# Kernel optimization log

Hardware: AMD Instinct MI355X
Metric: run time of the kernel (lower is better)

Reference implementation:

```python
import jax, jax.numpy as jnp
import numpy as np

N_ATOMS = 131072
N_EDGES = 524288
N_MOLS = 2048
D = 128      # n_atom_basis
F = 128      # n_filters
G = 50       # n_gaussians
T = 3        # interaction blocks
CUTOFF = 5.0
LOG2 = float(np.log(2.0))


def ssp(x):
    # shifted softplus: ln(0.5*e^x + 0.5) = softplus(x) - ln 2
    return jax.nn.softplus(x) - LOG2


def setup_inputs() -> dict:
    key = jax.random.key(0)
    ks = jax.random.split(key, 20)
    s = 0.05
    z = jax.random.randint(ks[0], (N_ATOMS,), 1, 100, dtype=jnp.int32)
    xyz = jax.random.normal(ks[1], (N_ATOMS, 3), dtype=jnp.float32) * 3.0
    a0 = jax.random.randint(ks[2], (N_EDGES,), 0, N_ATOMS, dtype=jnp.int32)
    off = jax.random.randint(ks[3], (N_EDGES,), 1, N_ATOMS, dtype=jnp.int32)
    a = jnp.stack([a0, (a0 + off) % N_ATOMS], axis=1)  # distinct endpoints
    mol_id = jnp.sort(jax.random.randint(ks[4], (N_ATOMS,), 0, N_MOLS, dtype=jnp.int32))
    emb = (jax.random.normal(ks[5], (100, D)) * s).at[0].set(0.0)  # padding_idx=0
    return dict(
        xyz=xyz,
        emb=emb,
        fw1=jax.random.normal(ks[6], (T, G, F)) * s,
        fb1=jnp.zeros((T, F)),
        fw2=jax.random.normal(ks[7], (T, F, F)) * s,
        fb2=jnp.zeros((T, F)),
        win=jax.random.normal(ks[8], (T, D, F)) * s,
        wout1=jax.random.normal(ks[9], (T, F, D)) * s,
        bout1=jnp.zeros((T, D)),
        wout2=jax.random.normal(ks[10], (T, D, D)) * s,
        bout2=jnp.zeros((T, D)),
        wa1=jax.random.normal(ks[11], (D, D // 2)) * s,
        ba1=jnp.zeros((D // 2,)),
        wa2=jax.random.normal(ks[12], (D // 2, 1)) * s,
        ba2=jnp.zeros((1,)),
        z=z, a=a, mol_id=mol_id,
    )


def reference(xyz, emb, fw1, fb1, fw2, fb2, win, wout1, bout1, wout2, bout2,
              wa1, ba1, wa2, ba2, z, a, mol_id):
    r = emb[z]                                            # [N, D] atom embeddings
    # edge distances: e = ||xyz[a0] - xyz[a1]||  -> [E, 1]
    d = jnp.sqrt(((xyz[a[:, 0]] - xyz[a[:, 1]]) ** 2).sum(-1))[:, None]
    # Gaussian smearing on [0, cutoff]
    offsets = jnp.linspace(0.0, CUTOFF, G)
    width = offsets[1] - offsets[0]
    g = jnp.exp((-0.5 / width ** 2) * (d - offsets) ** 2)  # [E, G]
    # smooth cosine cutoff (cutoff_soft)
    C = 0.5 * (jnp.cos(d * jnp.pi / CUTOFF) + 1.0)          # [E, 1]
    for t in range(T):
        # continuous filter network on edge features
        W = ssp(g @ fw1[t] + fb1[t]) @ fw2[t] + fb2[t]      # [E, F]
        W = W * C
        h = r @ win[t]                                      # in2f, no bias [N, F]
        # symmetric gather-filter-scatter over undirected edge list
        y = jnp.zeros_like(h)
        y = y.at[a[:, 0]].add(h[a[:, 1]] * W)
        y = y.at[a[:, 1]].add(h[a[:, 0]] * W)
        dr = ssp(y @ wout1[t] + bout1[t]) @ wout2[t] + bout2[t]
        r = r + dr                                          # residual update
    # atomwise energy head
    r = ssp(r @ wa1 + ba1) @ wa2 + ba2                      # [N, 1]
    # per-molecule sum pooling (torch.split + sum)
    return jax.ops.segment_sum(r, mol_id, num_segments=N_MOLS)  # [N_MOLS, 1]
```

## Files before the change

kernel.cpp:

```cpp
#include <hip/hip_runtime.h>
#include <hip/hip_bf16.h>

#define N_ATOMS 131072
#define N_EDGES 524288
#define N_MOLS  2048
#define DD      128
#define FF      128
#define GG      50
#define TT      3

typedef __hip_bfloat16 bf16;
typedef __attribute__((ext_vector_type(8))) short short8;
typedef __attribute__((ext_vector_type(4))) float floatx4;

__device__ __forceinline__ float b2f(bf16 v) { return __bfloat162float(v); }
__device__ __forceinline__ bf16  f2b(float v) { return __float2bfloat16(v); }

__device__ __forceinline__ unsigned short f2bu(float f) {
    unsigned u = __float_as_uint(f);
    u += 0x7fff + ((u >> 16) & 1);
    return (unsigned short)(u >> 16);
}
__device__ __forceinline__ bf16 f2b_fast(float f) {
    union { unsigned short u; bf16 b; } c; c.u = f2bu(f); return c.b;
}
__device__ __forceinline__ unsigned int pk2(float lo, float hi) {
    return ((unsigned)f2bu(hi) << 16) | f2bu(lo);
}

__device__ __forceinline__ unsigned short b2us(bf16 v) {
    union { bf16 b; unsigned short u; } c; c.b = v; return c.u;
}

__device__ __forceinline__ float2 up2(unsigned int u) {
    float2 f;
    f.x = __uint_as_float(u << 16);
    f.y = __uint_as_float(u & 0xffff0000u);
    return f;
}

__device__ __forceinline__ float sspf(float x) {
    float e = __expf(-fabsf(x));
    return fmaxf(x, 0.f) + __logf(1.f + e) - 0.69314718056f;
}

template <int NCT>
__device__ __forceinline__ void mfma_half(const bf16* A, const bf16* B,
                                          floatx4 (&acc)[2][NCT],
                                          int kA, int wave, int q, int ln) {
#pragma unroll
    for (int k0 = 0; k0 < 64; k0 += 32) {
        short8 a0 = *(const short8*)(A + (wave * 32 + ln) * 136 + kA + k0 + q * 8);
        short8 a1 = *(const short8*)(A + (wave * 32 + 16 + ln) * 136 + kA + k0 + q * 8);
#pragma unroll
        for (int ct = 0; ct < NCT; ct++) {
            short8 b = *(const short8*)(B + (ct * 16 + ln) * 72 + k0 + q * 8);
            acc[0][ct] = __builtin_amdgcn_mfma_f32_16x16x32_bf16(a0, b, acc[0][ct], 0, 0, 0);
            acc[1][ct] = __builtin_amdgcn_mfma_f32_16x16x32_bf16(a1, b, acc[1][ct], 0, 0, 0);
        }
    }
}

template <int NCT>
__device__ __forceinline__ void mfma64(const bf16* A, const bf16* B,
                                       floatx4 (&acc)[NCT],
                                       int kA, int wave, int q, int ln) {
#pragma unroll
    for (int k0 = 0; k0 < 64; k0 += 32) {
        short8 a = *(const short8*)(A + (wave * 16 + ln) * 136 + kA + k0 + q * 8);
#pragma unroll
        for (int ct = 0; ct < NCT; ct++) {
            short8 b = *(const short8*)(B + (ct * 16 + ln) * 72 + k0 + q * 8);
            acc[ct] = __builtin_amdgcn_mfma_f32_16x16x32_bf16(a, b, acc[ct], 0, 0, 0);
        }
    }
}

__device__ __forceinline__ void stage_b(bf16* B, const bf16* WT, int k0,
                                        int nrows, int ldk, int tid) {
    for (int i = tid; i < nrows * 8; i += 256) {
        int n = i >> 3, kc = i & 7;
        *(short8*)(B + n * 72 + kc * 8) =
            *(const short8*)(WT + n * ldk + k0 + kc * 8);
    }
}

__global__ __launch_bounds__(256) void k_init(const float* __restrict__ emb,
                                              const int* __restrict__ z,
                                              float* __restrict__ r) {
    int idx = blockIdx.x * 256 + threadIdx.x;
    int atom = idx >> 7, col = idx & 127;
    r[idx] = emb[z[atom] * DD + col];
}

__global__ __launch_bounds__(256) void k_dist(const float* __restrict__ xyz,
                                              const int* __restrict__ a,
                                              float* __restrict__ dArr,
                                              float* __restrict__ cArr,
                                              float* __restrict__ molE) {
    int e = blockIdx.x * 256 + threadIdx.x;
    if (e < N_MOLS) molE[e] = 0.f;
    int A0 = a[2 * e], A1 = a[2 * e + 1];
    float dx = xyz[3 * A0]     - xyz[3 * A1];
    float dy = xyz[3 * A0 + 1] - xyz[3 * A1 + 1];
    float dz = xyz[3 * A0 + 2] - xyz[3 * A1 + 2];
    float d = sqrtf(dx * dx + dy * dy + dz * dz);
    dArr[e] = d;
    cArr[e] = 0.5f * (__cosf(d * 0.6283185307179586f) + 1.f);
}

__global__ __launch_bounds__(256) void k_wt(const float* __restrict__ fw1,
                                            const float* __restrict__ fw2,
                                            const float* __restrict__ win,
                                            const float* __restrict__ wout1,
                                            const float* __restrict__ wout2,
                                            const float* __restrict__ wa1,
                                            bf16* __restrict__ fw1T, bf16* __restrict__ fw2T,
                                            bf16* __restrict__ winT, bf16* __restrict__ wout1T,
                                            bf16* __restrict__ wout2T, bf16* __restrict__ wa1T) {
    int idx = blockIdx.x * 256 + threadIdx.x;
    if (idx < 3 * 128 * 64) {
        int t = idx / 8192, j = idx % 8192;
        int n = j >> 6, k = j & 63;
        fw1T[idx] = (k < GG) ? f2b(fw1[t * GG * FF + k * FF + n]) : f2b(0.f);
        return;
    }
    idx -= 3 * 128 * 64;
    if (idx < 3 * 16384) { int t = idx / 16384, j = idx % 16384; int n = j >> 7, k = j & 127;
        fw2T[idx] = f2b(fw2[t * 16384 + k * 128 + n]); return; }
    idx -= 3 * 16384;
    if (idx < 3 * 16384) { int t = idx / 16384, j = idx % 16384; int n = j >> 7, k = j & 127;
        winT[idx] = f2b(win[t * 16384 + k * 128 + n]); return; }
    idx -= 3 * 16384;
    if (idx < 3 * 16384) { int t = idx / 16384, j = idx % 16384; int n = j >> 7, k = j & 127;
        wout1T[idx] = f2b(wout1[t * 16384 + k * 128 + n]); return; }
    idx -= 3 * 16384;
    if (idx < 3 * 16384) { int t = idx / 16384, j = idx % 16384; int n = j >> 7, k = j & 127;
        wout2T[idx] = f2b(wout2[t * 16384 + k * 128 + n]); return; }
    idx -= 3 * 16384;
    if (idx < 64 * 128) { int n = idx >> 7, k = idx & 127;
        wa1T[idx] = f2b(wa1[k * 64 + n]); return; }
}

__global__ __launch_bounds__(256) void k_zero(int* __restrict__ p, int n) {
    int i = blockIdx.x * 256 + threadIdx.x;
    if (i < n) p[i] = 0;
}

__global__ __launch_bounds__(256) void k_count(const int* __restrict__ a,
                                               int* __restrict__ counts) {
    int e = blockIdx.x * 256 + threadIdx.x;
    atomicAdd(&counts[a[2 * e]], 1);
    atomicAdd(&counts[a[2 * e + 1]], 1);
}

__global__ __launch_bounds__(256) void k_scan(int* __restrict__ counts,
                                              int* __restrict__ ptr) {
    __shared__ int part[256];
    int tid = threadIdx.x;
    const int CH = N_ATOMS / 256;
    int base = tid * CH;
    int s = 0;
    for (int i = 0; i < CH; i++) s += counts[base + i];
    part[tid] = s;
    __syncthreads();
    if (tid == 0) {
        int acc = 0;
        for (int i = 0; i < 256; i++) { int v = part[i]; part[i] = acc; acc += v; }
    }
    __syncthreads();
    int run = part[tid];
    for (int i = 0; i < CH; i++) {
        int v = counts[base + i];
        ptr[base + i] = run;
        counts[base + i] = run;
        run += v;
    }
    if (tid == 255) ptr[N_ATOMS] = run;
}

__global__ __launch_bounds__(256) void k_fill(const int* __restrict__ a,
                                              int* __restrict__ cursor,
                                              int* __restrict__ adj) {
    int e = blockIdx.x * 256 + threadIdx.x;
    int A0 = a[2 * e], A1 = a[2 * e + 1];
    int p0 = atomicAdd(&cursor[A0], 1);
    adj[2 * p0] = e; adj[2 * p0 + 1] = A1;
    int p1 = atomicAdd(&cursor[A1], 1);
    adj[2 * p1] = e; adj[2 * p1 + 1] = A0;
}


__global__ __launch_bounds__(256, 4) void k_h64(const float* __restrict__ r,
                                                const bf16* __restrict__ winT_t,
                                                bf16* __restrict__ h) {
    __shared__ __align__(16) bf16 A[64][136];
    __shared__ __align__(16) bf16 B[128][72];
    int tid = threadIdx.x, n0 = blockIdx.x * 64;
    for (int i = tid; i < 64 * 32; i += 256) {
        int row = i >> 5, c4 = (i & 31) * 4;
        float4 v = *(const float4*)(r + (size_t)(n0 + row) * DD + c4);
        uint2 p; p.x = pk2(v.x, v.y); p.y = pk2(v.z, v.w);
        *(uint2*)(&A[row][c4]) = p;
    }
    stage_b(&B[0][0], winT_t, 0, 128, 128, tid);
    __syncthreads();
    int wave = tid >> 6, lane = tid & 63, q = lane >> 4, ln = lane & 15;
    floatx4 acc[8];
#pragma unroll
    for (int j = 0; j < 8; j++) acc[j] = (floatx4){0.f, 0.f, 0.f, 0.f};
    mfma64<8>(&A[0][0], &B[0][0], acc, 0, wave, q, ln);
    __syncthreads();
    stage_b(&B[0][0], winT_t, 64, 128, 128, tid);
    __syncthreads();
    mfma64<8>(&A[0][0], &B[0][0], acc, 64, wave, q, ln);
#pragma unroll
    for (int ct = 0; ct < 8; ct++)
#pragma unroll
        for (int rg = 0; rg < 4; rg++) {
            int row = wave * 16 + q * 4 + rg, col = ct * 16 + ln;
            A[row][col] = f2b_fast(acc[ct][rg]);
        }
    __syncthreads();
    for (int i = tid; i < 64 * 16; i += 256) {
        int row = i >> 4, seg = i & 15;
        *(uint4*)(h + (size_t)(n0 + row) * FF + seg * 8) =
            *(const uint4*)(&A[row][seg * 8]);
    }
}

__global__ __launch_bounds__(256, 4) void k_edge_w64(const float* __restrict__ dArr,
                                                     const float* __restrict__ cArr,
                                                     const bf16* __restrict__ fw1T_t,
                                                     const float* __restrict__ fb1_t,
                                                     const bf16* __restrict__ fw2T_t,
                                                     const float* __restrict__ fb2_t,
                                                     bf16* __restrict__ Wt) {
    __shared__ __align__(16) bf16 A[64][136];
    __shared__ __align__(16) bf16 B[128][72];
    __shared__ float dS[64], cS[64], b1S[128], b2S[128];
    int tid = threadIdx.x, e0 = blockIdx.x * 64;
    if (tid < 64) { dS[tid] = dArr[e0 + tid]; cS[tid] = cArr[e0 + tid]; }
    if (tid < 128) { b1S[tid] = fb1_t[tid]; b2S[tid] = fb2_t[tid]; }
    stage_b(&B[0][0], fw1T_t, 0, 128, 64, tid);
    __syncthreads();
    const float width = 5.0f / 49.0f;
    const float coeff = -0.5f / (width * width);
    for (int idx = tid; idx < 64 * 32; idx += 256) {
        int i = idx >> 5, kp = (idx & 31) * 2;
        float d = dS[i];
        float t0 = d - (float)kp * width;
        float t1 = d - (float)(kp + 1) * width;
        float v0 = (kp < GG)     ? __expf(coeff * t0 * t0) : 0.f;
        float v1 = (kp + 1 < GG) ? __expf(coeff * t1 * t1) : 0.f;
        *(unsigned int*)(&A[i][kp]) = pk2(v0, v1);
    }
    __syncthreads();
    int wave = tid >> 6, lane = tid & 63, q = lane >> 4, ln = lane & 15;
    floatx4 acc[8];
#pragma unroll
    for (int j = 0; j < 8; j++) acc[j] = (floatx4){0.f, 0.f, 0.f, 0.f};
    mfma64<8>(&A[0][0], &B[0][0], acc, 0, wave, q, ln);
#pragma unroll
    for (int ct = 0; ct < 8; ct++)
#pragma unroll
        for (int rg = 0; rg < 4; rg++) {
            int row = wave * 16 + q * 4 + rg, col = ct * 16 + ln;
            A[row][col] = f2b_fast(sspf(acc[ct][rg] + b1S[col]));
        }
    __syncthreads();
    stage_b(&B[0][0], fw2T_t, 0, 128, 128, tid);
    __syncthreads();
#pragma unroll
    for (int j = 0; j < 8; j++) acc[j] = (floatx4){0.f, 0.f, 0.f, 0.f};
    mfma64<8>(&A[0][0], &B[0][0], acc, 0, wave, q, ln);
    __syncthreads();
    stage_b(&B[0][0], fw2T_t, 64, 128, 128, tid);
    __syncthreads();
    mfma64<8>(&A[0][0], &B[0][0], acc, 64, wave, q, ln);
#pragma unroll
    for (int ct = 0; ct < 8; ct++)
#pragma unroll
        for (int rg = 0; rg < 4; rg++) {
            int row = wave * 16 + q * 4 + rg, col = ct * 16 + ln;
            A[row][col] = f2b_fast((acc[ct][rg] + b2S[col]) * cS[row]);
        }
    __syncthreads();
    for (int i = tid; i < 64 * 16; i += 256) {
        int row = i >> 4, seg = i & 15;
        *(uint4*)(Wt + (size_t)(e0 + row) * FF + seg * 8) =
            *(const uint4*)(&A[row][seg * 8]);
    }
}

__global__ __launch_bounds__(256, 4) void k_gather_node64(const int* __restrict__ ptr,
                                                          const int* __restrict__ adj,
                                                          const bf16* __restrict__ Wt,
                                                          const bf16* __restrict__ h,
                                                          const bf16* __restrict__ wout1T_t,
                                                          const float* __restrict__ bo1_t,
                                                          const bf16* __restrict__ wout2T_t,
                                                          const float* __restrict__ bo2_t,
                                                          float* __restrict__ r) {
    __shared__ __align__(16) bf16 A[64][136];
    __shared__ __align__(16) bf16 B[128][72];
    __shared__ float b1S[128], b2S[128];
    int tid = threadIdx.x, n0 = blockIdx.x * 64;
    if (tid < 128) { b1S[tid] = bo1_t[tid]; b2S[tid] = bo2_t[tid]; }
    int wave = tid >> 6, lane = tid & 63;
    int seg = lane & 15;
    int rg  = lane >> 4;
    for (int k = 0; k < 16; k++) {
        int row = wave * 16 + k;
        int atom = n0 + row;
        int beg = ptr[atom], end = ptr[atom + 1];
        float ac[8];
#pragma unroll
        for (int j = 0; j < 8; j++) ac[j] = 0.f;
        for (int s0 = beg; s0 < end; s0 += 4) {
            int slot = s0 + rg;
            if (slot < end) {
                int2 eo = *(const int2*)(adj + 2 * slot);
                uint4 wv = *(const uint4*)(Wt + (size_t)eo.x * FF + seg * 8);
                uint4 hv = *(const uint4*)(h + (size_t)eo.y * FF + seg * 8);
                float2 w0 = up2(wv.x), h0 = up2(hv.x);
                float2 w1 = up2(wv.y), h1 = up2(hv.y);
                float2 w2 = up2(wv.z), h2 = up2(hv.z);
                float2 w3 = up2(wv.w), h3 = up2(hv.w);
                ac[0] = fmaf(w0.x, h0.x, ac[0]); ac[1] = fmaf(w0.y, h0.y, ac[1]);
                ac[2] = fmaf(w1.x, h1.x, ac[2]); ac[3] = fmaf(w1.y, h1.y, ac[3]);
                ac[4] = fmaf(w2.x, h2.x, ac[4]); ac[5] = fmaf(w2.y, h2.y, ac[5]);
                ac[6] = fmaf(w3.x, h3.x, ac[6]); ac[7] = fmaf(w3.y, h3.y, ac[7]);
            }
        }
#pragma unroll
        for (int j = 0; j < 8; j++) {
            float v = ac[j];
            v += __shfl_down(v, 32);
            v += __shfl_down(v, 16);
            ac[j] = v;
        }
        if (rg == 0) {
            uint4 o;
            o.x = pk2(ac[0], ac[1]);
            o.y = pk2(ac[2], ac[3]);
            o.z = pk2(ac[4], ac[5]);
            o.w = pk2(ac[6], ac[7]);
            *(uint4*)(&A[row][seg * 8]) = o;
        }
    }
    stage_b(&B[0][0], wout1T_t, 0, 128, 128, tid);
    __syncthreads();
    int q = lane >> 4, ln = lane & 15;
    floatx4 acc[8];
#pragma unroll
    for (int j = 0; j < 8; j++) acc[j] = (floatx4){0.f, 0.f, 0.f, 0.f};
    mfma64<8>(&A[0][0], &B[0][0], acc, 0, wave, q, ln);
    __syncthreads();
    stage_b(&B[0][0], wout1T_t, 64, 128, 128, tid);
    __syncthreads();
    mfma64<8>(&A[0][0], &B[0][0], acc, 64, wave, q, ln);
#pragma unroll
    for (int ct = 0; ct < 8; ct++)
#pragma unroll
        for (int rgi = 0; rgi < 4; rgi++) {
            int row = wave * 16 + q * 4 + rgi, col = ct * 16 + ln;
            A[row][col] = f2b_fast(sspf(acc[ct][rgi] + b1S[col]));
        }
    __syncthreads();
    stage_b(&B[0][0], wout2T_t, 0, 128, 128, tid);
    __syncthreads();
#pragma unroll
    for (int j = 0; j < 8; j++) acc[j] = (floatx4){0.f, 0.f, 0.f, 0.f};
    mfma64<8>(&A[0][0], &B[0][0], acc, 0, wave, q, ln);
    __syncthreads();
    stage_b(&B[0][0], wout2T_t, 64, 128, 128, tid);
    __syncthreads();
    mfma64<8>(&A[0][0], &B[0][0], acc, 64, wave, q, ln);
#pragma unroll
    for (int ct = 0; ct < 8; ct++)
#pragma unroll
        for (int rgi = 0; rgi < 4; rgi++) {
            int row = wave * 16 + q * 4 + rgi, col = ct * 16 + ln;
            size_t off = (size_t)(n0 + row) * DD + col;
            r[off] += acc[ct][rgi] + b2S[col];
        }
}

__global__ __launch_bounds__(256) void k_h(const float* __restrict__ r,
                                           const bf16* __restrict__ winT_t,
                                           bf16* __restrict__ h,
                                           float* __restrict__ y) {
    __shared__ __align__(16) bf16 A[128][136];
    __shared__ __align__(16) bf16 B[128][72];
    int tid = threadIdx.x, n0 = blockIdx.x * 128;
    for (int i = tid; i < 128 * 32; i += 256) {
        int row = i >> 5, c4 = (i & 31) * 4;
        float4 v = *(const float4*)(r + (size_t)(n0 + row) * DD + c4);
        A[row][c4]     = f2b(v.x);
        A[row][c4 + 1] = f2b(v.y);
        A[row][c4 + 2] = f2b(v.z);
        A[row][c4 + 3] = f2b(v.w);
        *(float4*)(y + (size_t)(n0 + row) * FF + c4) = (float4){0.f, 0.f, 0.f, 0.f};
    }
    stage_b(&B[0][0], winT_t, 0, 128, 128, tid);
    __syncthreads();
    int wave = tid >> 6, lane = tid & 63, q = lane >> 4, ln = lane & 15;
    floatx4 acc[2][8];
#pragma unroll
    for (int i = 0; i < 2; i++)
#pragma unroll
        for (int j = 0; j < 8; j++) acc[i][j] = (floatx4){0.f, 0.f, 0.f, 0.f};
    mfma_half<8>(&A[0][0], &B[0][0], acc, 0, wave, q, ln);
    __syncthreads();
    stage_b(&B[0][0], winT_t, 64, 128, 128, tid);
    __syncthreads();
    mfma_half<8>(&A[0][0], &B[0][0], acc, 64, wave, q, ln);
#pragma unroll
    for (int rt = 0; rt < 2; rt++)
#pragma unroll
        for (int ct = 0; ct < 8; ct++)
#pragma unroll
            for (int rg = 0; rg < 4; rg++) {
                int row = wave * 32 + rt * 16 + q * 4 + rg, col = ct * 16 + ln;
                h[(size_t)(n0 + row) * FF + col] = f2b(acc[rt][ct][rg]);
            }
}

__global__ __launch_bounds__(256) void k_edge(const float* __restrict__ dArr,
                                              const float* __restrict__ cArr,
                                              const int* __restrict__ a,
                                              const bf16* __restrict__ fw1T_t,
                                              const float* __restrict__ fb1_t,
                                              const bf16* __restrict__ fw2T_t,
                                              const float* __restrict__ fb2_t,
                                              const bf16* __restrict__ h,
                                              float* __restrict__ y) {
    __shared__ __align__(16) bf16 A[128][136];
    __shared__ __align__(16) bf16 B[128][72];
    __shared__ float dS[128], cS[128], b1S[128], b2S[128];
    __shared__ int a0S[128], a1S[128];
    int tid = threadIdx.x, e0 = blockIdx.x * 128;
    if (tid < 128) {
        int e = e0 + tid;
        dS[tid] = dArr[e]; cS[tid] = cArr[e];
        a0S[tid] = a[2 * e]; a1S[tid] = a[2 * e + 1];
        b1S[tid] = fb1_t[tid]; b2S[tid] = fb2_t[tid];
    }
    stage_b(&B[0][0], fw1T_t, 0, 128, 64, tid);
    __syncthreads();
    const float width = 5.0f / 49.0f;
    const float coeff = -0.5f / (width * width);
    for (int idx = tid; idx < 128 * 64; idx += 256) {
        int i = idx >> 6, k = idx & 63;
        float v = 0.f;
        if (k < GG) { float t = dS[i] - (float)k * width; v = __expf(coeff * t * t); }
        A[i][k] = f2b(v);
    }
    __syncthreads();
    int wave = tid >> 6, lane = tid & 63, q = lane >> 4, ln = lane & 15;
    floatx4 acc[2][8];
#pragma unroll
    for (int i = 0; i < 2; i++)
#pragma unroll
        for (int j = 0; j < 8; j++) acc[i][j] = (floatx4){0.f, 0.f, 0.f, 0.f};
    mfma_half<8>(&A[0][0], &B[0][0], acc, 0, wave, q, ln);
#pragma unroll
    for (int rt = 0; rt < 2; rt++)
#pragma unroll
        for (int ct = 0; ct < 8; ct++)
#pragma unroll
            for (int rg = 0; rg < 4; rg++) {
                int row = wave * 32 + rt * 16 + q * 4 + rg, col = ct * 16 + ln;
                A[row][col] = f2b(sspf(acc[rt][ct][rg] + b1S[col]));
            }
    __syncthreads();
    stage_b(&B[0][0], fw2T_t, 0, 128, 128, tid);
    __syncthreads();
#pragma unroll
    for (int i = 0; i < 2; i++)
#pragma unroll
        for (int j = 0; j < 8; j++) acc[i][j] = (floatx4){0.f, 0.f, 0.f, 0.f};
    mfma_half<8>(&A[0][0], &B[0][0], acc, 0, wave, q, ln);
    __syncthreads();
    stage_b(&B[0][0], fw2T_t, 64, 128, 128, tid);
    __syncthreads();
    mfma_half<8>(&A[0][0], &B[0][0], acc, 64, wave, q, ln);
#pragma unroll
    for (int rt = 0; rt < 2; rt++)
#pragma unroll
        for (int ct = 0; ct < 8; ct++)
#pragma unroll
            for (int rg = 0; rg < 4; rg++) {
                int row = wave * 32 + rt * 16 + q * 4 + rg, col = ct * 16 + ln;
                float w = (acc[rt][ct][rg] + b2S[col]) * cS[row];
                int A0 = a0S[row], A1 = a1S[row];
                float h0 = b2f(h[A0 * FF + col]);
                float h1 = b2f(h[A1 * FF + col]);
                atomicAdd(&y[A0 * FF + col], h1 * w);
                atomicAdd(&y[A1 * FF + col], h0 * w);
            }
}

__global__ __launch_bounds__(256) void k_node(const float* __restrict__ y,
                                              const bf16* __restrict__ wout1T_t,
                                              const float* __restrict__ bo1_t,
                                              const bf16* __restrict__ wout2T_t,
                                              const float* __restrict__ bo2_t,
                                              float* __restrict__ r) {
    __shared__ __align__(16) bf16 A[128][136];
    __shared__ __align__(16) bf16 B[128][72];
    __shared__ float b1S[128], b2S[128];
    int tid = threadIdx.x, n0 = blockIdx.x * 128;
    if (tid < 128) { b1S[tid] = bo1_t[tid]; b2S[tid] = bo2_t[tid]; }
    for (int idx = tid; idx < 128 * 128; idx += 256) {
        int row = idx >> 7, col = idx & 127;
        A[row][col] = f2b(y[(size_t)(n0 + row) * FF + col]);
    }
    stage_b(&B[0][0], wout1T_t, 0, 128, 128, tid);
    __syncthreads();
    int wave = tid >> 6, lane = tid & 63, q = lane >> 4, ln = lane & 15;
    floatx4 acc[2][8];
#pragma unroll
    for (int i = 0; i < 2; i++)
#pragma unroll
        for (int j = 0; j < 8; j++) acc[i][j] = (floatx4){0.f, 0.f, 0.f, 0.f};
    mfma_half<8>(&A[0][0], &B[0][0], acc, 0, wave, q, ln);
    __syncthreads();
    stage_b(&B[0][0], wout1T_t, 64, 128, 128, tid);
    __syncthreads();
    mfma_half<8>(&A[0][0], &B[0][0], acc, 64, wave, q, ln);
#pragma unroll
    for (int rt = 0; rt < 2; rt++)
#pragma unroll
        for (int ct = 0; ct < 8; ct++)
#pragma unroll
            for (int rg = 0; rg < 4; rg++) {
                int row = wave * 32 + rt * 16 + q * 4 + rg, col = ct * 16 + ln;
                A[row][col] = f2b(sspf(acc[rt][ct][rg] + b1S[col]));
            }
    __syncthreads();
    stage_b(&B[0][0], wout2T_t, 0, 128, 128, tid);
    __syncthreads();
#pragma unroll
    for (int i = 0; i < 2; i++)
#pragma unroll
        for (int j = 0; j < 8; j++) acc[i][j] = (floatx4){0.f, 0.f, 0.f, 0.f};
    mfma_half<8>(&A[0][0], &B[0][0], acc, 0, wave, q, ln);
    __syncthreads();
    stage_b(&B[0][0], wout2T_t, 64, 128, 128, tid);
    __syncthreads();
    mfma_half<8>(&A[0][0], &B[0][0], acc, 64, wave, q, ln);
#pragma unroll
    for (int rt = 0; rt < 2; rt++)
#pragma unroll
        for (int ct = 0; ct < 8; ct++)
#pragma unroll
            for (int rg = 0; rg < 4; rg++) {
                int row = wave * 32 + rt * 16 + q * 4 + rg, col = ct * 16 + ln;
                size_t off = (size_t)(n0 + row) * DD + col;
                r[off] += acc[rt][ct][rg] + b2S[col];
            }
}

__global__ __launch_bounds__(256) void k_head(const float* __restrict__ r,
                                              const bf16* __restrict__ wa1T,
                                              const float* __restrict__ ba1,
                                              const float* __restrict__ wa2,
                                              const float* __restrict__ ba2,
                                              const int* __restrict__ mol,
                                              float* __restrict__ molE) {
    __shared__ __align__(16) bf16 A[128][136];
    __shared__ __align__(16) bf16 B[64][72];
    __shared__ __align__(16) bf16 U[128][72];
    __shared__ float wa2S[64], ba1S[64];
    int tid = threadIdx.x, n0 = blockIdx.x * 128;
    if (tid < 64) { wa2S[tid] = wa2[tid]; ba1S[tid] = ba1[tid]; }
    for (int i = tid; i < 128 * 32; i += 256) {
        int row = i >> 5, c4 = (i & 31) * 4;
        float4 v = *(const float4*)(r + (size_t)(n0 + row) * DD + c4);
        uint2 p; p.x = pk2(v.x, v.y); p.y = pk2(v.z, v.w);
        *(uint2*)(&A[row][c4]) = p;
    }
    stage_b(&B[0][0], wa1T, 0, 64, 128, tid);
    __syncthreads();
    int wave = tid >> 6, lane = tid & 63, q = lane >> 4, ln = lane & 15;
    floatx4 acc[2][4];
#pragma unroll
    for (int i = 0; i < 2; i++)
#pragma unroll
        for (int j = 0; j < 4; j++) acc[i][j] = (floatx4){0.f, 0.f, 0.f, 0.f};
    mfma_half<4>(&A[0][0], &B[0][0], acc, 0, wave, q, ln);
    __syncthreads();
    stage_b(&B[0][0], wa1T, 64, 64, 128, tid);
    __syncthreads();
    mfma_half<4>(&A[0][0], &B[0][0], acc, 64, wave, q, ln);
#pragma unroll
    for (int rt = 0; rt < 2; rt++)
#pragma unroll
        for (int ct = 0; ct < 4; ct++)
#pragma unroll
            for (int rg = 0; rg < 4; rg++) {
                int row = wave * 32 + rt * 16 + q * 4 + rg, col = ct * 16 + ln;
                U[row][col] = f2b_fast(acc[rt][ct][rg] + ba1S[col]);
            }
    __syncthreads();
    if (tid < 128) {
        float s = ba2[0];
#pragma unroll
        for (int j = 0; j < 64; j++) s += sspf(b2f(U[tid][j])) * wa2S[j];
        atomicAdd(&molE[mol[n0 + tid]], s);
    }
}

__global__ __launch_bounds__(256) void k_out(const float* __restrict__ molE,
                                             float* __restrict__ out) {
    int i = blockIdx.x * 256 + threadIdx.x;
    out[i] = molE[i];
}

extern "C" void kernel_launch(void* const* d_in, const int* in_sizes, int n_in,
                              void* d_out, int out_size, void* d_ws, size_t ws_size,
                              hipStream_t stream) {
    const float* xyz   = (const float*)d_in[0];
    const float* emb   = (const float*)d_in[1];
    const float* fw1   = (const float*)d_in[2];
    const float* fb1   = (const float*)d_in[3];
    const float* fw2   = (const float*)d_in[4];
    const float* fb2   = (const float*)d_in[5];
    const float* win   = (const float*)d_in[6];
    const float* wout1 = (const float*)d_in[7];
    const float* bout1 = (const float*)d_in[8];
    const float* wout2 = (const float*)d_in[9];
    const float* bout2 = (const float*)d_in[10];
    const float* wa1   = (const float*)d_in[11];
    const float* ba1   = (const float*)d_in[12];
    const float* wa2   = (const float*)d_in[13];
    const float* ba2   = (const float*)d_in[14];
    const int*  z     = (const int*)d_in[15];
    const int*  a     = (const int*)d_in[16];
    const int*  mol   = (const int*)d_in[17];

    char* ws = (char*)d_ws;
    float* r    = (float*)ws; ws += (size_t)N_ATOMS * DD * 4;
    bf16*  h    = (bf16*) ws; ws += (size_t)N_ATOMS * FF * 2;
    float* dA   = (float*)ws; ws += (size_t)N_EDGES * 4;
    float* cA   = (float*)ws; ws += (size_t)N_EDGES * 4;
    float* molE = (float*)ws; ws += (size_t)N_MOLS * 4;
    bf16*  fw1T   = (bf16*)ws; ws += 3 * 128 * 64 * 2;
    bf16*  fw2T   = (bf16*)ws; ws += 3 * 128 * 128 * 2;
    bf16*  winT   = (bf16*)ws; ws += 3 * 128 * 128 * 2;
    bf16*  wout1T = (bf16*)ws; ws += 3 * 128 * 128 * 2;
    bf16*  wout2T = (bf16*)ws; ws += 3 * 128 * 128 * 2;
    bf16*  wa1T   = (bf16*)ws; ws += 64 * 128 * 2;
    char*  csr_base = ws;
    int*   ptr    = (int*)ws;  ws += 524304;
    int*   cursor = (int*)ws;  ws += (size_t)N_ATOMS * 4;
    int*   adj    = (int*)ws;  ws += (size_t)2 * N_EDGES * 2 * 4;
    bf16*  Wt     = (bf16*)ws; ws += (size_t)N_EDGES * FF * 2;
    size_t need = (size_t)(ws - (char*)d_ws);

    k_init<<<N_ATOMS * DD / 256, 256, 0, stream>>>(emb, z, r);
    k_dist<<<N_EDGES / 256, 256, 0, stream>>>(xyz, a, dA, cA, molE);
    k_wt<<<896, 256, 0, stream>>>(fw1, fw2, win, wout1, wout2, wa1,
                                  fw1T, fw2T, winT, wout1T, wout2T, wa1T);

    if (ws_size >= need) {
        k_zero<<<(N_ATOMS + 255) / 256, 256, 0, stream>>>(cursor, N_ATOMS);
        k_count<<<N_EDGES / 256, 256, 0, stream>>>(a, cursor);
        k_scan<<<1, 256, 0, stream>>>(cursor, ptr);
        k_fill<<<N_EDGES / 256, 256, 0, stream>>>(a, cursor, adj);
        for (int t = 0; t < TT; t++) {
            k_h64<<<N_ATOMS / 64, 256, 0, stream>>>(r, winT + t * 16384, h);
            k_edge_w64<<<N_EDGES / 64, 256, 0, stream>>>(dA, cA,
                                                         fw1T + t * 8192, fb1 + t * FF,
                                                         fw2T + t * 16384, fb2 + t * FF, Wt);
            k_gather_node64<<<N_ATOMS / 64, 256, 0, stream>>>(ptr, adj, Wt, h,
                                                              wout1T + t * 16384, bout1 + t * DD,
                                                              wout2T + t * 16384, bout2 + t * DD, r);
        }
    } else {
        float* y = (float*)csr_base;
        for (int t = 0; t < TT; t++) {
            k_h<<<N_ATOMS / 128, 256, 0, stream>>>(r, winT + t * 16384, h, y);
            k_edge<<<N_EDGES / 128, 256, 0, stream>>>(dA, cA, a,
                                                      fw1T + t * 8192, fb1 + t * FF,
                                                      fw2T + t * 16384, fb2 + t * FF, h, y);
            k_node<<<N_ATOMS / 128, 256, 0, stream>>>(y, wout1T + t * 16384, bout1 + t * DD,
                                                      wout2T + t * 16384, bout2 + t * DD, r);
        }
    }
    k_head<<<N_ATOMS / 128, 256, 0, stream>>>(r, wa1T, ba1, wa2, ba2, mol, molE);
    k_out<<<N_MOLS / 256, 256, 0, stream>>>(molE, (float*)d_out);
}
```

Before: 1.135 ms.

## Sort edges by source atom and fuse h and edge-filter kernels

```diff
diff --git a/kernel.cpp b/kernel.cpp
--- a/kernel.cpp
+++ b/kernel.cpp
@@ -28,10 +28,6 @@
     return ((unsigned)f2bu(hi) << 16) | f2bu(lo);
 }
 
-__device__ __forceinline__ unsigned short b2us(bf16 v) {
-    union { bf16 b; unsigned short u; } c; c.b = v; return c.u;
-}
-
 __device__ __forceinline__ float2 up2(unsigned int u) {
     float2 f;
     f.x = __uint_as_float(u << 16);
@@ -42,6 +38,17 @@
 __device__ __forceinline__ float sspf(float x) {
     float e = __expf(-fabsf(x));
     return fmaxf(x, 0.f) + __logf(1.f + e) - 0.69314718056f;
+}
+
+__device__ __forceinline__ void fma8(float* ac, uint4 wv, uint4 hv) {
+    float2 w0 = up2(wv.x), h0 = up2(hv.x);
+    float2 w1 = up2(wv.y), h1 = up2(hv.y);
+    float2 w2 = up2(wv.z), h2 = up2(hv.z);
+    float2 w3 = up2(wv.w), h3 = up2(hv.w);
+    ac[0] = fmaf(w0.x, h0.x, ac[0]); ac[1] = fmaf(w0.y, h0.y, ac[1]);
+    ac[2] = fmaf(w1.x, h1.x, ac[2]); ac[3] = fmaf(w1.y, h1.y, ac[3]);
+    ac[4] = fmaf(w2.x, h2.x, ac[4]); ac[5] = fmaf(w2.y, h2.y, ac[5]);
+    ac[6] = fmaf(w3.x, h3.x, ac[6]); ac[7] = fmaf(w3.y, h3.y, ac[7]);
 }
 
 template <int NCT>
@@ -147,11 +154,14 @@
     if (i < n) p[i] = 0;
 }
 
-__global__ __launch_bounds__(256) void k_count(const int* __restrict__ a,
-                                               int* __restrict__ counts) {
+__global__ __launch_bounds__(256) void k_count2(const int* __restrict__ a,
+                                                int* __restrict__ cntA,
+                                                int* __restrict__ cnt1,
+                                                float* __restrict__ molE) {
     int e = blockIdx.x * 256 + threadIdx.x;
-    atomicAdd(&counts[a[2 * e]], 1);
-    atomicAdd(&counts[a[2 * e + 1]], 1);
+    if (e < N_MOLS) molE[e] = 0.f;
+    atomicAdd(&cntA[a[2 * e]], 1);
+    atomicAdd(&cnt1[a[2 * e + 1]], 1);
 }
 
 __global__ __launch_bounds__(256) void k_scan(int* __restrict__ counts,
@@ -179,122 +189,156 @@
     if (tid == 255) ptr[N_ATOMS] = run;
 }
 
-__global__ __launch_bounds__(256) void k_fill(const int* __restrict__ a,
-                                              int* __restrict__ cursor,
-                                              int* __restrict__ adj) {
+__global__ __launch_bounds__(256) void k_permA(const float* __restrict__ xyz,
+                                               const int* __restrict__ a,
+                                               int* __restrict__ cursorA,
+                                               int* __restrict__ cursor1,
+                                               float* __restrict__ dAp,
+                                               float* __restrict__ cAp,
+                                               int* __restrict__ a1s,
+                                               int* __restrict__ adj1) {
     int e = blockIdx.x * 256 + threadIdx.x;
     int A0 = a[2 * e], A1 = a[2 * e + 1];
-    int p0 = atomicAdd(&cursor[A0], 1);
-    adj[2 * p0] = e; adj[2 * p0 + 1] = A1;
-    int p1 = atomicAdd(&cursor[A1], 1);
-    adj[2 * p1] = e; adj[2 * p1 + 1] = A0;
-}
-
-
-__global__ __launch_bounds__(256, 4) void k_h64(const float* __restrict__ r,
-                                                const bf16* __restrict__ winT_t,
-                                                bf16* __restrict__ h) {
-    __shared__ __align__(16) bf16 A[64][136];
-    __shared__ __align__(16) bf16 B[128][72];
-    int tid = threadIdx.x, n0 = blockIdx.x * 64;
+    float dx = xyz[3 * A0]     - xyz[3 * A1];
+    float dy = xyz[3 * A0 + 1] - xyz[3 * A1 + 1];
+    float dz = xyz[3 * A0 + 2] - xyz[3 * A1 + 2];
+    float d = sqrtf(dx * dx + dy * dy + dz * dz);
+    int newe = atomicAdd(&cursorA[A0], 1);
+    dAp[newe] = d;
+    cAp[newe] = 0.5f * (__cosf(d * 0.6283185307179586f) + 1.f);
+    a1s[newe] = A1;
+    int slot = atomicAdd(&cursor1[A1], 1);
+    adj1[2 * slot] = newe;
+    adj1[2 * slot + 1] = A0;
+}
+
+struct SmemHE {
+    bf16 A[64][136];
+    bf16 B[128][72];
+    float dS[64], cS[64], b1S[128], b2S[128];
+};
+
+__device__ __forceinline__ void h_part(SmemHE& sm, int blk,
+                                       const float* __restrict__ r,
+                                       const bf16* __restrict__ winT_t,
+                                       bf16* __restrict__ h) {
+    int tid = threadIdx.x, n0 = blk * 64;
     for (int i = tid; i < 64 * 32; i += 256) {
         int row = i >> 5, c4 = (i & 31) * 4;
         float4 v = *(const float4*)(r + (size_t)(n0 + row) * DD + c4);
         uint2 p; p.x = pk2(v.x, v.y); p.y = pk2(v.z, v.w);
-        *(uint2*)(&A[row][c4]) = p;
-    }
-    stage_b(&B[0][0], winT_t, 0, 128, 128, tid);
+        *(uint2*)(&sm.A[row][c4]) = p;
+    }
+    stage_b(&sm.B[0][0], winT_t, 0, 128, 128, tid);
     __syncthreads();
     int wave = tid >> 6, lane = tid & 63, q = lane >> 4, ln = lane & 15;
     floatx4 acc[8];
 #pragma unroll
     for (int j = 0; j < 8; j++) acc[j] = (floatx4){0.f, 0.f, 0.f, 0.f};
-    mfma64<8>(&A[0][0], &B[0][0], acc, 0, wave, q, ln);
-    __syncthreads();
-    stage_b(&B[0][0], winT_t, 64, 128, 128, tid);
-    __syncthreads();
-    mfma64<8>(&A[0][0], &B[0][0], acc, 64, wave, q, ln);
+    mfma64<8>(&sm.A[0][0], &sm.B[0][0], acc, 0, wave, q, ln);
+    __syncthreads();
+    stage_b(&sm.B[0][0], winT_t, 64, 128, 128, tid);
+    __syncthreads();
+    mfma64<8>(&sm.A[0][0], &sm.B[0][0], acc, 64, wave, q, ln);
 #pragma unroll
     for (int ct = 0; ct < 8; ct++)
 #pragma unroll
         for (int rg = 0; rg < 4; rg++) {
             int row = wave * 16 + q * 4 + rg, col = ct * 16 + ln;
-            A[row][col] = f2b_fast(acc[ct][rg]);
+            sm.A[row][col] = f2b_fast(acc[ct][rg]);
         }
     __syncthreads();
     for (int i = tid; i < 64 * 16; i += 256) {
         int row = i >> 4, seg = i & 15;
         *(uint4*)(h + (size_t)(n0 + row) * FF + seg * 8) =
-            *(const uint4*)(&A[row][seg * 8]);
-    }
-}
-
-__global__ __launch_bounds__(256, 4) void k_edge_w64(const float* __restrict__ dArr,
-                                                     const float* __restrict__ cArr,
-                                                     const bf16* __restrict__ fw1T_t,
-                                                     const float* __restrict__ fb1_t,
-                                                     const bf16* __restrict__ fw2T_t,
-                                                     const float* __restrict__ fb2_t,
-                                                     bf16* __restrict__ Wt) {
-    __shared__ __align__(16) bf16 A[64][136];
-    __shared__ __align__(16) bf16 B[128][72];
-    __shared__ float dS[64], cS[64], b1S[128], b2S[128];
-    int tid = threadIdx.x, e0 = blockIdx.x * 64;
-    if (tid < 64) { dS[tid] = dArr[e0 + tid]; cS[tid] = cArr[e0 + tid]; }
-    if (tid < 128) { b1S[tid] = fb1_t[tid]; b2S[tid] = fb2_t[tid]; }
-    stage_b(&B[0][0], fw1T_t, 0, 128, 64, tid);
+            *(const uint4*)(&sm.A[row][seg * 8]);
+    }
+}
+
+__device__ __forceinline__ void edge_part(SmemHE& sm, int blk,
+                                          const float* __restrict__ dAp,
+                                          const float* __restrict__ cAp,
+                                          const bf16* __restrict__ fw1T_t,
+                                          const float* __restrict__ fb1_t,
+                                          const bf16* __restrict__ fw2T_t,
+                                          const float* __restrict__ fb2_t,
+                                          bf16* __restrict__ Wt) {
+    int tid = threadIdx.x, e0 = blk * 64;
+    if (tid < 64) { sm.dS[tid] = dAp[e0 + tid]; sm.cS[tid] = cAp[e0 + tid]; }
+    if (tid < 128) { sm.b1S[tid] = fb1_t[tid]; sm.b2S[tid] = fb2_t[tid]; }
+    stage_b(&sm.B[0][0], fw1T_t, 0, 128, 64, tid);
     __syncthreads();
     const float width = 5.0f / 49.0f;
     const float coeff = -0.5f / (width * width);
     for (int idx = tid; idx < 64 * 32; idx += 256) {
         int i = idx >> 5, kp = (idx & 31) * 2;
-        float d = dS[i];
+        float d = sm.dS[i];
         float t0 = d - (float)kp * width;
         float t1 = d - (float)(kp + 1) * width;
         float v0 = (kp < GG)     ? __expf(coeff * t0 * t0) : 0.f;
         float v1 = (kp + 1 < GG) ? __expf(coeff * t1 * t1) : 0.f;
-        *(unsigned int*)(&A[i][kp]) = pk2(v0, v1);
+        *(unsigned int*)(&sm.A[i][kp]) = pk2(v0, v1);
     }
     __syncthreads();
     int wave = tid >> 6, lane = tid & 63, q = lane >> 4, ln = lane & 15;
     floatx4 acc[8];
 #pragma unroll
     for (int j = 0; j < 8; j++) acc[j] = (floatx4){0.f, 0.f, 0.f, 0.f};
-    mfma64<8>(&A[0][0], &B[0][0], acc, 0, wave, q, ln);
+    mfma64<8>(&sm.A[0][0], &sm.B[0][0], acc, 0, wave, q, ln);
 #pragma unroll
     for (int ct = 0; ct < 8; ct++)
 #pragma unroll
         for (int rg = 0; rg < 4; rg++) {
             int row = wave * 16 + q * 4 + rg, col = ct * 16 + ln;
-            A[row][col] = f2b_fast(sspf(acc[ct][rg] + b1S[col]));
-        }
-    __syncthreads();
-    stage_b(&B[0][0], fw2T_t, 0, 128, 128, tid);
+            sm.A[row][col] = f2b_fast(sspf(acc[ct][rg] + sm.b1S[col]));
+        }
+    __syncthreads();
+    stage_b(&sm.B[0][0], fw2T_t, 0, 128, 128, tid);
     __syncthreads();
 #pragma unroll
     for (int j = 0; j < 8; j++) acc[j] = (floatx4){0.f, 0.f, 0.f, 0.f};
-    mfma64<8>(&A[0][0], &B[0][0], acc, 0, wave, q, ln);
-    __syncthreads();
-    stage_b(&B[0][0], fw2T_t, 64, 128, 128, tid);
-    __syncthreads();
-    mfma64<8>(&A[0][0], &B[0][0], acc, 64, wave, q, ln);
+    mfma64<8>(&sm.A[0][0], &sm.B[0][0], acc, 0, wave, q, ln);
+    __syncthreads();
+    stage_b(&sm.B[0][0], fw2T_t, 64, 128, 128, tid);
+    __syncthreads();
+    mfma64<8>(&sm.A[0][0], &sm.B[0][0], acc, 64, wave, q, ln);
 #pragma unroll
     for (int ct = 0; ct < 8; ct++)
 #pragma unroll
         for (int rg = 0; rg < 4; rg++) {
             int row = wave * 16 + q * 4 + rg, col = ct * 16 + ln;
-            A[row][col] = f2b_fast((acc[ct][rg] + b2S[col]) * cS[row]);
+            sm.A[row][col] = f2b_fast((acc[ct][rg] + sm.b2S[col]) * sm.cS[row]);
         }
     __syncthreads();
     for (int i = tid; i < 64 * 16; i += 256) {
         int row = i >> 4, seg = i & 15;
         *(uint4*)(Wt + (size_t)(e0 + row) * FF + seg * 8) =
-            *(const uint4*)(&A[row][seg * 8]);
-    }
-}
-
-__global__ __launch_bounds__(256, 4) void k_gather_node64(const int* __restrict__ ptr,
-                                                          const int* __restrict__ adj,
+            *(const uint4*)(&sm.A[row][seg * 8]);
+    }
+}
+
+__global__ __launch_bounds__(256, 4) void k_he(const float* __restrict__ r,
+                                               const bf16* __restrict__ winT_t,
+                                               bf16* __restrict__ h,
+                                               const float* __restrict__ dAp,
+                                               const float* __restrict__ cAp,
+                                               const bf16* __restrict__ fw1T_t,
+                                               const float* __restrict__ fb1_t,
+                                               const bf16* __restrict__ fw2T_t,
+                                               const float* __restrict__ fb2_t,
+                                               bf16* __restrict__ Wt) {
+    __shared__ SmemHE sm;
+    int bi = blockIdx.x;
+    if (bi % 5 == 0)
+        h_part(sm, bi / 5, r, winT_t, h);
+    else
+        edge_part(sm, bi - bi / 5 - 1, dAp, cAp, fw1T_t, fb1_t, fw2T_t, fb2_t, Wt);
+}
+
+__global__ __launch_bounds__(256, 4) void k_gather_node64(const int* __restrict__ baseA,
+                                                          const int* __restrict__ a1s,
+                                                          const int* __restrict__ ptr1,
+                                                          const int* __restrict__ adj1,
                                                           const bf16* __restrict__ Wt,
                                                           const bf16* __restrict__ h,
                                                           const bf16* __restrict__ wout1T_t,
@@ -307,31 +351,34 @@
     __shared__ float b1S[128], b2S[128];
     int tid = threadIdx.x, n0 = blockIdx.x * 64;
     if (tid < 128) { b1S[tid] = bo1_t[tid]; b2S[tid] = bo2_t[tid]; }
+    stage_b(&B[0][0], wout1T_t, 0, 128, 128, tid);
     int wave = tid >> 6, lane = tid & 63;
     int seg = lane & 15;
     int rg  = lane >> 4;
     for (int k = 0; k < 16; k++) {
         int row = wave * 16 + k;
         int atom = n0 + row;
-        int beg = ptr[atom], end = ptr[atom + 1];
+        int s0 = baseA[atom] + rg, e0 = baseA[atom + 1];
+        int s1 = ptr1[atom] + rg, e1 = ptr1[atom + 1];
         float ac[8];
 #pragma unroll
         for (int j = 0; j < 8; j++) ac[j] = 0.f;
-        for (int s0 = beg; s0 < end; s0 += 4) {
-            int slot = s0 + rg;
-            if (slot < end) {
-                int2 eo = *(const int2*)(adj + 2 * slot);
-                uint4 wv = *(const uint4*)(Wt + (size_t)eo.x * FF + seg * 8);
-                uint4 hv = *(const uint4*)(h + (size_t)eo.y * FF + seg * 8);
-                float2 w0 = up2(wv.x), h0 = up2(hv.x);
-                float2 w1 = up2(wv.y), h1 = up2(hv.y);
-                float2 w2 = up2(wv.z), h2 = up2(hv.z);
-                float2 w3 = up2(wv.w), h3 = up2(hv.w);
-                ac[0] = fmaf(w0.x, h0.x, ac[0]); ac[1] = fmaf(w0.y, h0.y, ac[1]);
-                ac[2] = fmaf(w1.x, h1.x, ac[2]); ac[3] = fmaf(w1.y, h1.y, ac[3]);
-                ac[4] = fmaf(w2.x, h2.x, ac[4]); ac[5] = fmaf(w2.y, h2.y, ac[5]);
-                ac[6] = fmaf(w3.x, h3.x, ac[6]); ac[7] = fmaf(w3.y, h3.y, ac[7]);
+        while (s0 < e0 || s1 < e1) {
+            bool p0 = s0 < e0, p1 = s1 < e1;
+            uint4 wv0, hv0, wv1, hv1;
+            if (p0) {
+                int o0 = a1s[s0];
+                wv0 = *(const uint4*)(Wt + (size_t)s0 * FF + seg * 8);
+                hv0 = *(const uint4*)(h + (size_t)o0 * FF + seg * 8);
             }
+            if (p1) {
+                int2 eo = *(const int2*)(adj1 + 2 * s1);
+                wv1 = *(const uint4*)(Wt + (size_t)eo.x * FF + seg * 8);
+                hv1 = *(const uint4*)(h + (size_t)eo.y * FF + seg * 8);
+            }
+            if (p0) fma8(ac, wv0, hv0);
+            if (p1) fma8(ac, wv1, hv1);
+            s0 += 4; s1 += 4;
         }
 #pragma unroll
         for (int j = 0; j < 8; j++) {
@@ -349,7 +396,6 @@
             *(uint4*)(&A[row][seg * 8]) = o;
         }
     }
-    stage_b(&B[0][0], wout1T_t, 0, 128, 128, tid);
     __syncthreads();
     int q = lane >> 4, ln = lane & 15;
     floatx4 acc[8];
@@ -644,9 +690,9 @@
     char* ws = (char*)d_ws;
     float* r    = (float*)ws; ws += (size_t)N_ATOMS * DD * 4;
     bf16*  h    = (bf16*) ws; ws += (size_t)N_ATOMS * FF * 2;
-    float* dA   = (float*)ws; ws += (size_t)N_EDGES * 4;
-    float* cA   = (float*)ws; ws += (size_t)N_EDGES * 4;
     float* molE = (float*)ws; ws += (size_t)N_MOLS * 4;
+    float* dAp  = (float*)ws; ws += (size_t)N_EDGES * 4;
+    float* cAp  = (float*)ws; ws += (size_t)N_EDGES * 4;
     bf16*  fw1T   = (bf16*)ws; ws += 3 * 128 * 64 * 2;
     bf16*  fw2T   = (bf16*)ws; ws += 3 * 128 * 128 * 2;
     bf16*  winT   = (bf16*)ws; ws += 3 * 128 * 128 * 2;
@@ -654,36 +700,43 @@
     bf16*  wout2T = (bf16*)ws; ws += 3 * 128 * 128 * 2;
     bf16*  wa1T   = (bf16*)ws; ws += 64 * 128 * 2;
     char*  csr_base = ws;
-    int*   ptr    = (int*)ws;  ws += 524304;
-    int*   cursor = (int*)ws;  ws += (size_t)N_ATOMS * 4;
-    int*   adj    = (int*)ws;  ws += (size_t)2 * N_EDGES * 2 * 4;
-    bf16*  Wt     = (bf16*)ws; ws += (size_t)N_EDGES * FF * 2;
+    int*   baseA   = (int*)ws; ws += 524320;
+    int*   ptr1    = (int*)ws; ws += 524320;
+    int*   cursorA = (int*)ws; ws += (size_t)N_ATOMS * 4;
+    int*   cursor1 = (int*)ws; ws += (size_t)N_ATOMS * 4;
+    int*   a1s     = (int*)ws; ws += (size_t)N_EDGES * 4;
+    int*   adj1    = (int*)ws; ws += (size_t)2 * N_EDGES * 4;
+    bf16*  Wt      = (bf16*)ws; ws += (size_t)N_EDGES * FF * 2;
     size_t need = (size_t)(ws - (char*)d_ws);
 
     k_init<<<N_ATOMS * DD / 256, 256, 0, stream>>>(emb, z, r);
-    k_dist<<<N_EDGES / 256, 256, 0, stream>>>(xyz, a, dA, cA, molE);
     k_wt<<<896, 256, 0, stream>>>(fw1, fw2, win, wout1, wout2, wa1,
                                   fw1T, fw2T, winT, wout1T, wout2T, wa1T);
 
     if (ws_size >= need) {
-        k_zero<<<(N_ATOMS + 255) / 256, 256, 0, stream>>>(cursor, N_ATOMS);
-        k_count<<<N_EDGES / 256, 256, 0, stream>>>(a, cursor);
-        k_scan<<<1, 256, 0, stream>>>(cursor, ptr);
-        k_fill<<<N_EDGES / 256, 256, 0, stream>>>(a, cursor, adj);
+        k_zero<<<(N_ATOMS + 255) / 256, 256, 0, stream>>>(cursorA, N_ATOMS);
+        k_zero<<<(N_ATOMS + 255) / 256, 256, 0, stream>>>(cursor1, N_ATOMS);
+        k_count2<<<N_EDGES / 256, 256, 0, stream>>>(a, cursorA, cursor1, molE);
+        k_scan<<<1, 256, 0, stream>>>(cursorA, baseA);
+        k_scan<<<1, 256, 0, stream>>>(cursor1, ptr1);
+        k_permA<<<N_EDGES / 256, 256, 0, stream>>>(xyz, a, cursorA, cursor1,
+                                                   dAp, cAp, a1s, adj1);
         for (int t = 0; t < TT; t++) {
-            k_h64<<<N_ATOMS / 64, 256, 0, stream>>>(r, winT + t * 16384, h);
-            k_edge_w64<<<N_EDGES / 64, 256, 0, stream>>>(dA, cA,
-                                                         fw1T + t * 8192, fb1 + t * FF,
-                                                         fw2T + t * 16384, fb2 + t * FF, Wt);
-            k_gather_node64<<<N_ATOMS / 64, 256, 0, stream>>>(ptr, adj, Wt, h,
-                                                              wout1T + t * 16384, bout1 + t * DD,
-                                                              wout2T + t * 16384, bout2 + t * DD, r);
+            k_he<<<N_ATOMS / 64 + N_EDGES / 64, 256, 0, stream>>>(
+                r, winT + t * 16384, h, dAp, cAp,
+                fw1T + t * 8192, fb1 + t * FF,
+                fw2T + t * 16384, fb2 + t * FF, Wt);
+            k_gather_node64<<<N_ATOMS / 64, 256, 0, stream>>>(
+                baseA, a1s, ptr1, adj1, Wt, h,
+                wout1T + t * 16384, bout1 + t * DD,
+                wout2T + t * 16384, bout2 + t * DD, r);
         }
     } else {
         float* y = (float*)csr_base;
+        k_dist<<<N_EDGES / 256, 256, 0, stream>>>(xyz, a, dAp, cAp, molE);
         for (int t = 0; t < TT; t++) {
             k_h<<<N_ATOMS / 128, 256, 0, stream>>>(r, winT + t * 16384, h, y);
-            k_edge<<<N_EDGES / 128, 256, 0, stream>>>(dA, cA, a,
+            k_edge<<<N_EDGES / 128, 256, 0, stream>>>(dAp, cAp, a,
                                                       fw1T + t * 8192, fb1 + t * FF,
                                                       fw2T + t * 16384, fb2 + t * FF, h, y);
             k_node<<<N_ATOMS / 128, 256, 0, stream>>>(y, wout1T + t * 16384, bout1 + t * DD,
```

After: 1.161 ms. 2.4% more time.
